# Performance work log

Hardware: AMD Instinct MI355X
Metric: run time of the kernel (lower is better)

The kernel has to match this reference:

```python
import jax, jax.numpy as jnp
import numpy as np

HASH_PRIME = 5099  # primes[layer_id=0]
MIN_CAPACITY = 4


def setup_inputs() -> dict:
    key = jax.random.key(0)
    k1, k2, k3, k4, k5 = jax.random.split(key, 5)
    B, T, D, F, E = 8, 4096, 512, 1792, 64
    x = jax.random.normal(k1, (B, T, D), dtype=jnp.float32)
    token_ids = jax.random.randint(k2, (B, T), 0, 50257, dtype=jnp.int32)
    # Expert params stacked over E (random instead of the degenerate zero init)
    Wk = jax.random.normal(k3, (E, F, D), dtype=jnp.float32) * 0.02
    Wr = jax.random.normal(k4, (E, D, D), dtype=jnp.float32) * 0.02
    Wv = jax.random.normal(k5, (E, D, F), dtype=jnp.float32) * 0.02
    return {"x": x, "token_ids": token_ids, "Wk": Wk, "Wr": Wr, "Wv": Wv}


def reference(x, token_ids, Wk, Wr, Wv):
    B, T, D = x.shape
    E = Wk.shape[0]
    S = B * T
    # capacity_factor = 1, k = 1 -> capacity = ceil(S / E), at least min_capacity
    cap = max(MIN_CAPACITY, -(-S // E))

    tid = token_ids.reshape(S)
    e_idx = (tid % HASH_PRIME) % E                     # hash routing, top-1, gate weight 1.0

    onehot = jax.nn.one_hot(e_idx, E, dtype=jnp.int32)  # [S, E]
    rank = (jnp.cumsum(onehot, axis=0) * onehot).sum(axis=1)  # 1-based rank within expert
    pos = rank - 1                                      # slot index within expert
    kept = pos < cap                                    # capacity drop (first-come order)

    xf = x.reshape(S, D)
    pos_safe = jnp.where(kept, pos, cap)                # out-of-bounds -> dropped by scatter
    dispatched = jnp.zeros((E, cap, D), x.dtype).at[e_idx, pos_safe].set(xf, mode='drop')

    # RWKV expert FFN, batched over experts
    h = jnp.square(jax.nn.relu(jnp.einsum('ecd,efd->ecf', dispatched, Wk)))  # [E,C,F]
    kv = jnp.einsum('ecf,edf->ecd', h, Wv)                                   # [E,C,D]
    r = jax.nn.sigmoid(jnp.einsum('ecd,egd->ecg', dispatched, Wr))           # [E,C,D]
    expert_out = r * kv

    # combine: gather each token's slot; dropped tokens get zeros
    yf = expert_out[e_idx, jnp.minimum(pos, cap - 1)] * kept[:, None].astype(x.dtype)
    return yf.reshape(B, T, D)
```

## Files before the change

kernel.cpp:

```cpp
#include <hip/hip_runtime.h>
#include <hip/hip_fp16.h>

#define HASH_PRIME 5099
#define NE 64
#define ND 512
#define NF 1792
#define NS 32768
#define CAP 512

typedef unsigned short u16;
typedef __attribute__((ext_vector_type(8))) short bf16x8;
typedef __attribute__((ext_vector_type(4))) float f32x4;

__device__ __forceinline__ u16 f2bf(float f) {
  union { float f; unsigned u; } v; v.f = f;
  return (u16)((v.u + 0x7FFFu + ((v.u >> 16) & 1u)) >> 16);
}
__device__ __forceinline__ unsigned pkbf2(float a, float b) {
  return (unsigned)f2bf(a) | ((unsigned)f2bf(b) << 16);
}

__device__ __forceinline__ void gld16(const void* g, void* l) {
  __builtin_amdgcn_global_load_lds(
      (const __attribute__((address_space(1))) unsigned int*)(uintptr_t)g,
      (__attribute__((address_space(3))) unsigned int*)(uintptr_t)l,
      16, 0, 0);
}

__global__ __launch_bounds__(512) void route1(const int* __restrict__ tok,
                                              int* __restrict__ rank_local,
                                              int* __restrict__ hist) {
  __shared__ int se[512];
  __shared__ int h[NE];
  int b = blockIdx.x, t = threadIdx.x;
  int s = b * 512 + t;
  int e = (tok[s] % HASH_PRIME) % NE;
  se[t] = e;
  if (t < NE) h[t] = 0;
  __syncthreads();
  int cnt = 0;
  for (int j = 0; j < t; ++j) cnt += (se[j] == e);
  rank_local[s] = cnt;
  atomicAdd(&h[e], 1);
  __syncthreads();
  if (t < NE) hist[b * NE + t] = h[t];
}

__global__ __launch_bounds__(512) void route2(const int* __restrict__ tok,
                                              const int* __restrict__ rank_local,
                                              const int* __restrict__ hist,
                                              int* __restrict__ slot_src) {
  __shared__ int off[NE];
  int b = blockIdx.x, t = threadIdx.x;
  if (t < NE) {
    int o = 0;
    for (int bb = 0; bb < b; ++bb) o += hist[bb * NE + t];
    off[t] = o;
  }
  __syncthreads();
  int s = b * 512 + t;
  int e = (tok[s] % HASH_PRIME) % NE;
  int pos = off[e] + rank_local[s];
  if (pos < CAP) slot_src[e * CAP + pos] = s;
}

__global__ __launch_bounds__(256) void dispatchx(const float* __restrict__ x,
                                                 const int* __restrict__ slot_src,
                                                 u16* __restrict__ Xd) {
  int b = blockIdx.x;
  int t = threadIdx.x;
  int row = b * 4 + (t >> 6);
  int col = (t & 63) * 8;
  int s = slot_src[row];
  uint4 w = make_uint4(0u, 0u, 0u, 0u);
  if (s >= 0) {
    const float4* p = (const float4*)(x + (size_t)s * ND + col);
    float4 a = p[0], c = p[1];
    w.x = pkbf2(a.x, a.y); w.y = pkbf2(a.z, a.w);
    w.z = pkbf2(c.x, c.y); w.w = pkbf2(c.z, c.w);
  }
  *(uint4*)(Xd + (size_t)row * ND + col) = w;
}


#define GDECL \
  __shared__ u16 AsH[2 * 256 * 64]; \
  __shared__ u16 BsH[2 * 256 * 64]; \
  const int t = threadIdx.x; \
  const int l = t & 63; \
  const int w = t >> 6; \
  const int wm = w >> 2; \
  const int wn = w & 3; \
  const int lrow = l & 15; \
  const int kb = l >> 4; \
  const int rsw0_ = ((kb) ^ (l & 7)) * 8; \
  const int rsw1_ = ((4 + kb) ^ (l & 7)) * 8; \
  const int arow_ = w * 8 + (l >> 3); \
  const int asw_ = ((l & 7) ^ (l >> 3)) * 8; \
  const int brow_ = (t >> 7) * 64 + ((t >> 2) & 31); \
  const int bkq_ = t & 3; \
  const int bsa_ = ((bkq_ * 2) ^ (brow_ & 7)) * 8; \
  const int bsb_ = ((bkq_ * 2 + 1) ^ (brow_ & 7)) * 8;

#define GLDA(sl, rbase, ktS, abase, AST) do { \
  const u16* g_ = (abase) + (size_t)((rbase) + arow_) * (AST) + (size_t)(ktS) * 64 + asw_; \
  gld16(g_, (char*)AsH + (sl) * 32768 + (rbase) * 128 + t * 16); \
} while (0)

#define LOADB(dst, ktS, u, bbase, BST) do { \
  const float4* p_ = (const float4*)((bbase) + (size_t)(brow_ + (u) * 32) * (BST) + (size_t)(ktS) * 64 + bkq_ * 16); \
  dst[0] = p_[0]; dst[1] = p_[1]; dst[2] = p_[2]; dst[3] = p_[3]; \
} while (0)

#define WRB(sl, u, src) do { \
  uint4 w0_, w1_; \
  w0_.x = pkbf2(src[0].x, src[0].y); w0_.y = pkbf2(src[0].z, src[0].w); \
  w0_.z = pkbf2(src[1].x, src[1].y); w0_.w = pkbf2(src[1].z, src[1].w); \
  w1_.x = pkbf2(src[2].x, src[2].y); w1_.y = pkbf2(src[2].z, src[2].w); \
  w1_.z = pkbf2(src[3].x, src[3].y); w1_.w = pkbf2(src[3].z, src[3].w); \
  *(uint4*)&BsH[(sl) * 16384 + (brow_ + (u) * 32) * 64 + bsa_] = w0_; \
  *(uint4*)&BsH[(sl) * 16384 + (brow_ + (u) * 32) * 64 + bsb_] = w1_; \
} while (0)

#define RDA(mh, slotH) do { \
  _Pragma("unroll") for (int ml_ = 0; ml_ < 4; ++ml_) { \
    const int r_ = wm * 128 + ((mh) * 4 + ml_) * 16 + lrow; \
    af[ml_][0] = *(const bf16x8*)&AsH[(slotH) + r_ * 64 + rsw0_]; \
    af[ml_][1] = *(const bf16x8*)&AsH[(slotH) + r_ * 64 + rsw1_]; \
  } \
} while (0)

#define RDB(np, slotH) do { \
  _Pragma("unroll") for (int nl_ = 0; nl_ < 2; ++nl_) { \
    const int r_ = wn * 64 + ((np) * 2 + nl_) * 16 + lrow; \
    bf[nl_][0] = *(const bf16x8*)&BsH[(slotH) + r_ * 64 + rsw0_]; \
    bf[nl_][1] = *(const bf16x8*)&BsH[(slotH) + r_ * 64 + rsw1_]; \
  } \
} while (0)

#define MFMA16(mh, np) do { \
  _Pragma("unroll") for (int ml_ = 0; ml_ < 4; ++ml_) \
    _Pragma("unroll") for (int nl_ = 0; nl_ < 2; ++nl_) \
      _Pragma("unroll") for (int ks_ = 0; ks_ < 2; ++ks_) \
        acc[(mh) * 4 + ml_][(np) * 2 + nl_] = __builtin_amdgcn_mfma_f32_16x16x32_bf16( \
            af[ml_][ks_], bf[nl_][ks_], acc[(mh) * 4 + ml_][(np) * 2 + nl_], 0, 0, 0); \
} while (0)

#define FENCE() asm volatile("" ::: "memory")
#define BAR()  do { FENCE(); __builtin_amdgcn_s_barrier(); FENCE(); } while (0)
#define LGKM0() asm volatile("s_waitcnt lgkmcnt(0)" ::: "memory")
#define VMW(n) asm volatile("s_waitcnt vmcnt(" #n ")" ::: "memory")

#define GEMM_CORE(NKT, abase, AST, bbase, BST) \
  f32x4 acc[8][4]; \
  _Pragma("unroll") for (int m_ = 0; m_ < 8; ++m_) \
    _Pragma("unroll") for (int n_ = 0; n_ < 4; ++n_) \
      acc[m_][n_] = (f32x4){0.f, 0.f, 0.f, 0.f}; \
  bf16x8 af[4][2]; \
  float4 fq[4], fu1[4]; \
   \
  GLDA(0, 0, 0, abase, AST); GLDA(0, 128, 0, abase, AST); \
  GLDA(0, 64, 0, abase, AST); GLDA(0, 192, 0, abase, AST); \
  LOADB(fq, 0, 0, bbase, BST); \
  LOADB(fu1, 0, 1, bbase, BST); \
  WRB(0, 0, fq); \
  VMW(0); \
  LGKM0(); \
  BAR(); \
  _Pragma("unroll 2") \
  for (int kt = 0; kt < (NKT); ++kt) { \
    const int slot = kt & 1, ss_ = slot ^ 1; \
    const int slotH = slot * 16384; \
    const int ktS = (kt + 1 < (NKT)) ? kt + 1 : 0; \
    {  \
      bf16x8 bf[2][2]; \
      RDA(0, slotH); RDB(0, slotH); \
      GLDA(ss_, 0, ktS, abase, AST); GLDA(ss_, 128, ktS, abase, AST); \
      WRB(slot, 1, fu1);  \
      BAR(); LGKM0(); \
      __builtin_amdgcn_s_setprio(1); MFMA16(0, 0); __builtin_amdgcn_s_setprio(0); \
      BAR(); \
    } \
    {  \
      bf16x8 bf[2][2]; \
      RDB(1, slotH); \
      LOADB(fq, ktS, 0, bbase, BST); \
      BAR(); LGKM0(); \
      __builtin_amdgcn_s_setprio(1); MFMA16(0, 1); __builtin_amdgcn_s_setprio(0); \
      VMW(6);   \
      BAR(); \
    } \
    {  \
      bf16x8 bf[2][2]; \
      RDA(1, slotH); RDB(0, slotH); \
      LOADB(fu1, ktS, 1, bbase, BST); \
      BAR(); LGKM0(); \
      __builtin_amdgcn_s_setprio(1); MFMA16(1, 0); __builtin_amdgcn_s_setprio(0); \
      BAR(); \
    } \
    {  \
      bf16x8 bf[2][2]; \
      RDB(1, slotH); \
      GLDA(ss_, 64, ktS, abase, AST); GLDA(ss_, 192, ktS, abase, AST); \
      WRB(ss_, 0, fq);  \
      BAR(); LGKM0(); \
      __builtin_amdgcn_s_setprio(1); MFMA16(1, 1); __builtin_amdgcn_s_setprio(0); \
      VMW(10);  \
      BAR(); \
    } \
  } \
  VMW(0);

__global__ __launch_bounds__(512, 2) void g1(const u16* __restrict__ Xd,
                                             const float* __restrict__ Wk,
                                             u16* __restrict__ H) {
  GDECL
  const int wg = (blockIdx.x & 7) * 112 + (blockIdx.x >> 3);
  const int e = wg / 14, rem = wg % 14;
  const int m0 = (rem & 1) * 256;
  const int n0 = (rem >> 1) * 256;
  const u16*  abase = Xd + ((size_t)e * CAP + m0) * ND;
  const float* bbase = Wk + ((size_t)e * NF + n0) * ND;
  GEMM_CORE(8, abase, ND, bbase, ND)

  #pragma unroll
  for (int m = 0; m < 8; ++m) {
    #pragma unroll
    for (int i = 0; i < 4; ++i) {
      int r = m0 + wm * 128 + m * 16 + (l >> 4) * 4 + i;
      size_t base = ((size_t)e * CAP + r) * NF + n0 + wn * 64 + lrow;
      #pragma unroll
      for (int n = 0; n < 4; ++n) {
        float v = acc[m][n][i];
        v = v > 0.f ? v * v : 0.f;
        H[base + n * 16] = f2bf(v);
      }
    }
  }
}

__global__ __launch_bounds__(512, 2) void g2a(const u16* __restrict__ Xd,
                                              const float* __restrict__ Wr,
                                              __half* __restrict__ R) {
  GDECL
  const int wg = (blockIdx.x & 7) * 32 + (blockIdx.x >> 3);
  const int e = wg >> 2, rem = wg & 3;
  const int m0 = (rem & 1) * 256;
  const int n0 = (rem >> 1) * 256;
  const u16*  abase = Xd + ((size_t)e * CAP + m0) * ND;
  const float* bbase = Wr + ((size_t)e * ND + n0) * ND;
  GEMM_CORE(8, abase, ND, bbase, ND)

  #pragma unroll
  for (int m = 0; m < 8; ++m) {
    #pragma unroll
    for (int i = 0; i < 4; ++i) {
      int r = m0 + wm * 128 + m * 16 + (l >> 4) * 4 + i;
      size_t base = ((size_t)e * CAP + r) * ND + n0 + wn * 64 + lrow;
      #pragma unroll
      for (int n = 0; n < 4; ++n) {
        float s = 1.f / (1.f + __expf(-acc[m][n][i]));
        R[base + n * 16] = __float2half(s);
      }
    }
  }
}

__global__ __launch_bounds__(512, 2) void g2b(const u16* __restrict__ H,
                                              const float* __restrict__ Wv,
                                              const __half* __restrict__ R,
                                              const int* __restrict__ slot_src,
                                              float* __restrict__ out) {
  GDECL
  const int wg = (blockIdx.x & 7) * 32 + (blockIdx.x >> 3);
  const int e = wg >> 2, rem = wg & 3;
  const int m0 = (rem & 1) * 256;
  const int n0 = (rem >> 1) * 256;
  const u16*  abase = H  + ((size_t)e * CAP + m0) * NF;
  const float* bbase = Wv + ((size_t)e * ND + n0) * NF;
  GEMM_CORE(28, abase, NF, bbase, NF)

  #pragma unroll
  for (int m = 0; m < 8; ++m) {
    #pragma unroll
    for (int i = 0; i < 4; ++i) {
      int rl = m0 + wm * 128 + m * 16 + (l >> 4) * 4 + i;
      int s = slot_src[e * CAP + rl];
      if (s >= 0) {
        const __half* rp = R + ((size_t)e * CAP + rl) * ND + n0 + wn * 64 + lrow;
        float* op = out + (size_t)s * ND + n0 + wn * 64 + lrow;
        #pragma unroll
        for (int n = 0; n < 4; ++n) {
          op[n * 16] = __half2float(rp[n * 16]) * acc[m][n][i];
        }
      }
    }
  }
}

extern "C" void kernel_launch(void* const* d_in, const int* in_sizes, int n_in,
                              void* d_out, int out_size, void* d_ws, size_t ws_size,
                              hipStream_t stream) {
  const float* x   = (const float*)d_in[0];
  const int*   tok = (const int*)d_in[1];
  const float* Wk  = (const float*)d_in[2];
  const float* Wr  = (const float*)d_in[3];
  const float* Wv  = (const float*)d_in[4];
  float* out = (float*)d_out;

  char* ws = (char*)d_ws;
  int*    slot_src   = (int*)ws;
  int*    rank_local = (int*)(ws + 131072);
  int*    hist       = (int*)(ws + 262144);
  u16*    Xd         = (u16*)(ws + (1 << 20));
  __half* R          = (__half*)(ws + 34603008);
  u16*    Hbuf       = (u16*)(ws + 68157440);

  (void)hipMemsetAsync(d_out, 0, (size_t)out_size * sizeof(float), stream);
  (void)hipMemsetAsync(slot_src, 0xFF, NE * CAP * sizeof(int), stream);
  route1<<<64, 512, 0, stream>>>(tok, rank_local, hist);
  route2<<<64, 512, 0, stream>>>(tok, rank_local, hist, slot_src);
  dispatchx<<<NS / 4, 256, 0, stream>>>(x, slot_src, Xd);
  g1 <<<896, 512, 0, stream>>>(Xd, Wk, Hbuf);
  g2a<<<256, 512, 0, stream>>>(Xd, Wr, R);
  g2b<<<256, 512, 0, stream>>>(Hbuf, Wv, R, slot_src, out);
}
```

Baseline: 383.1 us.

## Restructure GEMM main loop from four to two phases with full B fragment reuse

The per-k-tile loop drops from four compute phases to two. In each phase all four B fragments are read from LDS once and used for a 4x4 block of MFMAs, so B fragments are no longer re-read from LDS and the number of barriers per iteration halves. Both halves of the next B tile are now loaded together and written to LDS together in the second phase, which changes the vmcnt wait counts. This raises register pressure (a larger bf array and both fq and fu1 live at once) at occupancy 2, and leaves less interleaving of global loads with MFMA work.

```diff
diff --git a/kernel.cpp b/kernel.cpp
--- a/kernel.cpp
+++ b/kernel.cpp
@@ -130,20 +130,20 @@
   } \
 } while (0)
 
-#define RDB(np, slotH) do { \
-  _Pragma("unroll") for (int nl_ = 0; nl_ < 2; ++nl_) { \
-    const int r_ = wn * 64 + ((np) * 2 + nl_) * 16 + lrow; \
-    bf[nl_][0] = *(const bf16x8*)&BsH[(slotH) + r_ * 64 + rsw0_]; \
-    bf[nl_][1] = *(const bf16x8*)&BsH[(slotH) + r_ * 64 + rsw1_]; \
+#define RDB4(slotH) do { \
+  _Pragma("unroll") for (int nf_ = 0; nf_ < 4; ++nf_) { \
+    const int r_ = wn * 64 + nf_ * 16 + lrow; \
+    bf[nf_][0] = *(const bf16x8*)&BsH[(slotH) + r_ * 64 + rsw0_]; \
+    bf[nf_][1] = *(const bf16x8*)&BsH[(slotH) + r_ * 64 + rsw1_]; \
   } \
 } while (0)
 
-#define MFMA16(mh, np) do { \
+#define MFMA32(mh) do { \
   _Pragma("unroll") for (int ml_ = 0; ml_ < 4; ++ml_) \
-    _Pragma("unroll") for (int nl_ = 0; nl_ < 2; ++nl_) \
+    _Pragma("unroll") for (int nf_ = 0; nf_ < 4; ++nf_) \
       _Pragma("unroll") for (int ks_ = 0; ks_ < 2; ++ks_) \
-        acc[(mh) * 4 + ml_][(np) * 2 + nl_] = __builtin_amdgcn_mfma_f32_16x16x32_bf16( \
-            af[ml_][ks_], bf[nl_][ks_], acc[(mh) * 4 + ml_][(np) * 2 + nl_], 0, 0, 0); \
+        acc[(mh) * 4 + ml_][nf_] = __builtin_amdgcn_mfma_f32_16x16x32_bf16( \
+            af[ml_][ks_], bf[nf_][ks_], acc[(mh) * 4 + ml_][nf_], 0, 0, 0); \
 } while (0)
 
 #define FENCE() asm volatile("" ::: "memory")
@@ -157,13 +157,14 @@
     _Pragma("unroll") for (int n_ = 0; n_ < 4; ++n_) \
       acc[m_][n_] = (f32x4){0.f, 0.f, 0.f, 0.f}; \
   bf16x8 af[4][2]; \
+  bf16x8 bf[4][2]; \
   float4 fq[4], fu1[4]; \
    \
   GLDA(0, 0, 0, abase, AST); GLDA(0, 128, 0, abase, AST); \
   GLDA(0, 64, 0, abase, AST); GLDA(0, 192, 0, abase, AST); \
   LOADB(fq, 0, 0, bbase, BST); \
   LOADB(fu1, 0, 1, bbase, BST); \
-  WRB(0, 0, fq); \
+  WRB(0, 0, fq); WRB(0, 1, fu1); \
   VMW(0); \
   LGKM0(); \
   BAR(); \
@@ -173,39 +174,22 @@
     const int slotH = slot * 16384; \
     const int ktS = (kt + 1 < (NKT)) ? kt + 1 : 0; \
     {  \
-      bf16x8 bf[2][2]; \
-      RDA(0, slotH); RDB(0, slotH); \
+      RDA(0, slotH); RDB4(slotH); \
       GLDA(ss_, 0, ktS, abase, AST); GLDA(ss_, 128, ktS, abase, AST); \
-      WRB(slot, 1, fu1);  \
+      LOADB(fq, ktS, 0, bbase, BST); \
+      LOADB(fu1, ktS, 1, bbase, BST); \
       BAR(); LGKM0(); \
-      __builtin_amdgcn_s_setprio(1); MFMA16(0, 0); __builtin_amdgcn_s_setprio(0); \
+      __builtin_amdgcn_s_setprio(1); MFMA32(0); __builtin_amdgcn_s_setprio(0); \
+      VMW(10);  \
       BAR(); \
     } \
     {  \
-      bf16x8 bf[2][2]; \
-      RDB(1, slotH); \
-      LOADB(fq, ktS, 0, bbase, BST); \
+      RDA(1, slotH); \
+      GLDA(ss_, 64, ktS, abase, AST); GLDA(ss_, 192, ktS, abase, AST); \
+      WRB(ss_, 0, fq); WRB(ss_, 1, fu1); \
       BAR(); LGKM0(); \
-      __builtin_amdgcn_s_setprio(1); MFMA16(0, 1); __builtin_amdgcn_s_setprio(0); \
-      VMW(6);   \
-      BAR(); \
-    } \
-    {  \
-      bf16x8 bf[2][2]; \
-      RDA(1, slotH); RDB(0, slotH); \
-      LOADB(fu1, ktS, 1, bbase, BST); \
-      BAR(); LGKM0(); \
-      __builtin_amdgcn_s_setprio(1); MFMA16(1, 0); __builtin_amdgcn_s_setprio(0); \
-      BAR(); \
-    } \
-    {  \
-      bf16x8 bf[2][2]; \
-      RDB(1, slotH); \
-      GLDA(ss_, 64, ktS, abase, AST); GLDA(ss_, 192, ktS, abase, AST); \
-      WRB(ss_, 0, fq);  \
-      BAR(); LGKM0(); \
-      __builtin_amdgcn_s_setprio(1); MFMA16(1, 1); __builtin_amdgcn_s_setprio(0); \
-      VMW(10);  \
+      __builtin_amdgcn_s_setprio(1); MFMA32(1); __builtin_amdgcn_s_setprio(0); \
+      VMW(2);  \
       BAR(); \
     } \
   } \
```

New measurement: 393.3 us. 1.03x slower.
